# Kernel optimization log

Measured on AMD Instinct MI355X. Metric: run time of the kernel, lower is better.

Reference implementation:

```python
import jax, jax.numpy as jnp
import numpy as np

B, S, T, E = 16, 512, 4096, 256  # batch, phone count, frame count, embed dim


def _pe(t, e):
    # sinusoidal positional encoding table [t, e], matches PositionalEncoding
    pos = jnp.arange(t, dtype=jnp.float32)[:, None]
    div = jnp.exp(jnp.arange(0, e, 2, dtype=jnp.float32) * (-np.log(10000.0) / e))
    pe = jnp.zeros((t, e), jnp.float32)
    pe = pe.at[:, 0::2].set(jnp.sin(pos * div))
    pe = pe.at[:, 1::2].set(jnp.cos(pos * div))
    return pe


def setup_inputs() -> dict:
    key = jax.random.key(0)
    ks = jax.random.split(key, 8)
    encoder_out = jax.random.normal(ks[0], (B, S, E), jnp.float32)
    # text_phone with adjacent values guaranteed distinct (even pos in [0,29), odd in [30,59))
    base = jax.random.randint(ks[1], (B, S), 0, 29)
    off = (jnp.arange(S) % 2) * 30
    text_phone = (base + off[None, :]).astype(jnp.int64)
    dur = T // S
    align_phone = jnp.repeat(text_phone, dur, axis=1)  # [B, T], consistent alignment
    pitch = jax.random.normal(ks[2], (B, T, 1), jnp.float32)
    beats = jax.random.randint(ks[3], (B, T, 1), 0, 2).astype(jnp.int64)
    # learned parameters
    W_pitch = jax.random.normal(ks[4], (1, E), jnp.float32) * 0.02   # fc_pitch
    b_pitch = jnp.zeros((E,), jnp.float32)
    emb_beats = jax.random.normal(ks[5], (2, E), jnp.float32) * 0.02
    W_pos = jax.random.normal(ks[6], (E, E), jnp.float32) * (1.0 / np.sqrt(E))  # fc_pos
    b_pos = jnp.zeros((E,), jnp.float32)
    return dict(encoder_out=encoder_out, align_phone=align_phone, text_phone=text_phone,
                pitch=pitch, beats=beats, W_pitch=W_pitch, b_pitch=b_pitch,
                emb_beats=emb_beats, W_pos=W_pos, b_pos=b_pos)


def _align_indices(align_phone, text_phone):
    # Vectorized version of the serial aligner loop: per batch, an index into
    # encoder_out that stays while align_phone matches the current text phone
    # and advances by 1 otherwise.
    Bb, Ss = text_phone.shape
    barange = jnp.arange(Bb)

    def step(idx, a_j):
        before = text_phone[barange, idx]
        new = jnp.where(a_j == before, idx, jnp.minimum(idx + 1, Ss - 1))
        return new, new

    idx0 = jnp.zeros((Bb,), jnp.int32)
    _, rest = jax.lax.scan(step, idx0, align_phone[:, 1:].T)  # [T-1, B]
    return jnp.concatenate([idx0[None, :], rest], axis=0).T  # [B, T]


def reference(encoder_out, align_phone, text_phone, pitch, beats,
              W_pitch, b_pitch, emb_beats, W_pos, b_pos):
    idx = _align_indices(align_phone, text_phone)                       # [B, T]
    aligner_out = jnp.take_along_axis(encoder_out, idx[:, :, None].astype(jnp.int32), axis=1)  # [B, T, E]
    pitch_emb = pitch @ W_pitch + b_pitch                               # fc_pitch(pitch)
    beat_emb = emb_beats[beats[..., 0]]                                 # emb_beats(beats.squeeze(-1))
    # pos(aligner_out.transpose(0,1)) then transpose back; dropout is identity in eval
    pos_encode = aligner_out + _pe(aligner_out.shape[1], aligner_out.shape[2])[None, :, :]
    pos_out = pos_encode @ W_pos + b_pos                                # fc_pos
    return aligner_out + pitch_emb + beat_emb + pos_out
```

## Files before the change

kernel.cpp:

```cpp
#include <hip/hip_runtime.h>
#include <hip/hip_bf16.h>
#include <math.h>

constexpr int B_ = 16, S_ = 512, T_ = 4096, E_ = 256;

typedef __attribute__((ext_vector_type(8))) short short8;
typedef __attribute__((ext_vector_type(4))) float f32x4;

constexpr size_t FLAGS_OFF = 0;
constexpr size_t WT_OFF    = 4096;

#define NEGC (-0.035977892f)

__device__ __forceinline__ unsigned pk_bf16(float a, float b) {
    __hip_bfloat162 h = __float22bfloat162_rn(make_float2(a, b));
    return *(unsigned*)&h;
}
__device__ __forceinline__ short bf16s(float x) {
    unsigned u = __float_as_uint(x);
    u += 0x7FFFu + ((u >> 16) & 1u);
    return (short)(u >> 16);
}

__global__ __launch_bounds__(256) void k_prep(
    const int* __restrict__ align, const int* __restrict__ text,
    const float* __restrict__ W,
    int* __restrict__ flags, short* __restrict__ wt)
{
    const int bid = blockIdx.x, tid = threadIdx.x;
    if (bid < 32) {
        __shared__ int f;
        if (tid == 0) f = 0;
        __syncthreads();
        const int base = (bid * 256 + tid) * 8;
        const int4 a0 = *(const int4*)(align + base);
        const int4 a1 = *(const int4*)(align + base + 4);
        const int av[8] = {a0.x, a0.y, a0.z, a0.w, a1.x, a1.y, a1.z, a1.w};
        int bad = 0;
#pragma unroll
        for (int m = 0; m < 8; ++m) {
            const int id = base + m;
            const int t = id & (T_ - 1), b = id >> 12;
            if (t > 0) {
                const int prev = (t - 1) >> 3;
                const int expct = (av[m] == text[b * S_ + prev]) ? prev : min(prev + 1, S_ - 1);
                if ((t >> 3) != expct) bad = 1;
            }
        }
        if (bad) f = 1;
        __syncthreads();
        if (tid == 0) flags[bid] = f;
    } else {
        const int kb = (bid - 32) * 16;
        short8 v0, v1;
#pragma unroll
        for (int j = 0; j < 8; ++j) v0[j] = bf16s(W[(kb + j) * E_ + tid]);
#pragma unroll
        for (int j = 0; j < 8; ++j) v1[j] = bf16s(W[(kb + 8 + j) * E_ + tid]);
        *(short8*)(wt + tid * E_ + kb)     = v0;
        *(short8*)(wt + tid * E_ + kb + 8) = v1;
    }
}

__global__ __launch_bounds__(256) void k_fused(
    const float* __restrict__ enc, const short* __restrict__ wt,
    const float* __restrict__ bpos,
    const float* __restrict__ pitch, const int* __restrict__ beats,
    const float* __restrict__ wpitch, const float* __restrict__ bpitch,
    const float* __restrict__ embb,
    const float* __restrict__ W, const int* __restrict__ align,
    const int* __restrict__ text, const int* __restrict__ flags,
    float* __restrict__ out)
{
    __shared__ __align__(16) short As[64 * 256];
    __shared__ __align__(16) short Bs[64 * 256];
    __shared__ float pl[32 * 68];
    __shared__ int idxl[16][32];

    const int tid = threadIdx.x;
    const int i0 = blockIdx.x * 4;
    const int n0 = blockIdx.y * 64;
    const int t0base = i0 * 8;

    const bool fb = __any(flags[tid & 31] != 0);
    if (fb) {
        if (tid < 16) {
            int i = 0;
            const int b = tid;
            if (i0 == 0) idxl[b][0] = 0;
            const int tmax = t0base + 32;
            for (int t = 1; t < tmax; ++t) {
                if (align[b * T_ + t] != text[b * S_ + i]) i = min(i + 1, S_ - 1);
                if (t >= t0base) idxl[b][t - t0base] = i;
            }
        }
        __syncthreads();
        for (int r = tid; r < 512; r += 256) {
            const int bq = r >> 5, tt = r & 31;
            const int t = t0base + tt;
            const int i = idxl[bq][tt];
            const float* erow = enc + (size_t)(bq * S_ + i) * E_;
            const float p = pitch[(size_t)bq * T_ + t];
            const int bt = beats[(size_t)bq * T_ + t];
            for (int cc = 0; cc < 64; ++cc) {
                const int col = n0 + cc;
                float acc = 0.f;
                for (int k2 = 0; k2 < 128; ++k2) {
                    const float d = __expf((float)(2 * k2) * NEGC);
                    float s, c;
                    __sincosf((float)t * d, &s, &c);
                    acc += (erow[2 * k2] + s) * W[(2 * k2) * E_ + col]
                         + (erow[2 * k2 + 1] + c) * W[(2 * k2 + 1) * E_ + col];
                }
                out[((size_t)bq * T_ + t) * E_ + col] =
                    erow[col] + acc + bpos[col] + p * wpitch[col] + bpitch[col]
                    + (bt ? embb[E_ + col] : embb[col]);
            }
        }
        return;
    }

    const int c4o = tid & 15, rg = tid >> 4;
    const int gc = n0 + 4 * c4o;
    const int j = rg & 3;
    const int t0 = t0base + j * 8;
    float4 pi0[4], pi1[4]; int4 bt0[4], bt1[4]; f32x4 e4[4];
#pragma unroll
    for (int p = 0; p < 4; ++p) {
        const int bq = (rg + p * 16) >> 2;
        const size_t prow = (size_t)bq * T_ + t0;
        pi0[p] = *(const float4*)(pitch + prow);
        pi1[p] = *(const float4*)(pitch + prow + 4);
        bt0[p] = *(const int4*)(beats + prow);
        bt1[p] = *(const int4*)(beats + prow + 4);
        e4[p]  = *(const f32x4*)(enc + (size_t)(bq * S_ + i0 + j) * E_ + gc);
    }
    const f32x4 wp4 = *(const f32x4*)(wpitch + gc);
    const f32x4 cst = *(const f32x4*)(bpitch + gc) + *(const f32x4*)(bpos + gc);
    const f32x4 be0 = *(const f32x4*)(embb + gc);
    const f32x4 be1 = *(const f32x4*)(embb + E_ + gc);

    {
        const int r = tid >> 2, c4 = tid & 3;
        const short* bp = wt + (size_t)(n0 + r) * E_;
#pragma unroll
        for (int jj = 0; jj < 8; ++jj) {
            const int seg = c4 + 4 * jj;
            short8 v = *(const short8*)(bp + seg * 8);
            *(short8*)&Bs[(r * 256 + seg * 8) ^ ((r & 7) << 3)] = v;
        }
    }
    {
        const int r = tid >> 3;
        const int c8 = tid & 7;
        const float tf = (float)(t0base + r);
#pragma unroll
        for (int jj = 0; jj < 4; ++jj) {
            const int seg = c8 * 4 + jj;
            union { short8 v; unsigned u[4]; } cv;
#pragma unroll
            for (int m = 0; m < 4; ++m) {
                const int j2 = seg * 4 + m;
                const float d = __expf((float)(2 * j2) * NEGC);
                float s, c;
                __sincosf(tf * d, &s, &c);
                cv.u[m] = pk_bf16(s, c);
            }
            *(short8*)&As[(r * 256 + seg * 8) ^ ((r & 7) << 3)] = cv.v;
        }
    }
    __syncthreads();

    const int wid = tid >> 6, lane = tid & 63;
    const int q = lane >> 4, c = lane & 15;

    {
        const int ar = (wid & 1) * 16 + c;
        const int br0 = (wid >> 1) * 32 + c, br1 = br0 + 16;
        f32x4 p0 = {0.f, 0.f, 0.f, 0.f}, p1 = {0.f, 0.f, 0.f, 0.f};
#pragma unroll
        for (int ks = 0; ks < 8; ++ks) {
            const int kidx = ks * 32 + q * 8;
            short8 a  = *(const short8*)&As[(ar * 256 + kidx) ^ ((ar & 7) << 3)];
            short8 b0 = *(const short8*)&Bs[(br0 * 256 + kidx) ^ ((br0 & 7) << 3)];
            short8 b1 = *(const short8*)&Bs[(br1 * 256 + kidx) ^ ((br1 & 7) << 3)];
            p0 = __builtin_amdgcn_mfma_f32_16x16x32_bf16(a, b0, p0, 0, 0, 0);
            p1 = __builtin_amdgcn_mfma_f32_16x16x32_bf16(a, b1, p1, 0, 0, 0);
        }
#pragma unroll
        for (int rr = 0; rr < 4; ++rr) {
            const int prw = (wid & 1) * 16 + q * 4 + rr;
            pl[prw * 68 + (wid >> 1) * 32 + c]      = p0[rr];
            pl[prw * 68 + (wid >> 1) * 32 + 16 + c] = p1[rr];
        }
    }
    __syncthreads();

    f32x4 pv[8];
    {
        const int r = tid >> 2, c4 = tid & 3;
        const float* ap = enc + (size_t)((r >> 2) * S_ + i0 + (r & 3)) * E_;
#pragma unroll
        for (int jj = 0; jj < 8; ++jj) {
            const int seg = c4 + 4 * jj;
            float4 f0 = *(const float4*)(ap + seg * 8);
            float4 f1 = *(const float4*)(ap + seg * 8 + 4);
            union { short8 v; unsigned u[4]; } cv;
            cv.u[0] = pk_bf16(f0.x, f0.y);
            cv.u[1] = pk_bf16(f0.z, f0.w);
            cv.u[2] = pk_bf16(f1.x, f1.y);
            cv.u[3] = pk_bf16(f1.z, f1.w);
            *(short8*)&As[(r * 256 + seg * 8) ^ ((r & 7) << 3)] = cv.v;
        }
#pragma unroll
        for (int d = 0; d < 8; ++d)
            pv[d] = *(const f32x4*)&pl[(j * 8 + d) * 68 + 4 * c4o];
    }
    __syncthreads();

    const int wm = (wid >> 1) << 5, wn = (wid & 1) << 5;
    f32x4 acc[2][2] = {{{0.f, 0.f, 0.f, 0.f}, {0.f, 0.f, 0.f, 0.f}},
                       {{0.f, 0.f, 0.f, 0.f}, {0.f, 0.f, 0.f, 0.f}}};
#pragma unroll
    for (int ks = 0; ks < 8; ++ks) {
        const int kidx = ks * 32 + q * 8;
        const int ra0 = wm + c, ra1 = wm + 16 + c;
        const int rb0 = wn + c, rb1 = wn + 16 + c;
        short8 a0 = *(const short8*)&As[(ra0 * 256 + kidx) ^ ((ra0 & 7) << 3)];
        short8 a1 = *(const short8*)&As[(ra1 * 256 + kidx) ^ ((ra1 & 7) << 3)];
        short8 b0 = *(const short8*)&Bs[(rb0 * 256 + kidx) ^ ((rb0 & 7) << 3)];
        short8 b1 = *(const short8*)&Bs[(rb1 * 256 + kidx) ^ ((rb1 & 7) << 3)];
        acc[0][0] = __builtin_amdgcn_mfma_f32_16x16x32_bf16(a0, b0, acc[0][0], 0, 0, 0);
        acc[0][1] = __builtin_amdgcn_mfma_f32_16x16x32_bf16(a0, b1, acc[0][1], 0, 0, 0);
        acc[1][0] = __builtin_amdgcn_mfma_f32_16x16x32_bf16(a1, b0, acc[1][0], 0, 0, 0);
        acc[1][1] = __builtin_amdgcn_mfma_f32_16x16x32_bf16(a1, b1, acc[1][1], 0, 0, 0);
    }

    __syncthreads();
    float* ew = (float*)As;
#pragma unroll
    for (int mt = 0; mt < 2; ++mt)
#pragma unroll
        for (int nh = 0; nh < 2; ++nh)
#pragma unroll
            for (int rr = 0; rr < 4; ++rr)
                ew[(wm + mt * 16 + q * 4 + rr) * 68 + wn + nh * 16 + c] = acc[mt][nh][rr];
    __syncthreads();

#pragma unroll
    for (int p = 0; p < 4; ++p) {
        const int lrow = rg + p * 16;
        const int bq = lrow >> 2;
        const f32x4 ewv = *(const f32x4*)&ew[lrow * 68 + 4 * c4o];
        const f32x4 base = ewv + e4[p] + cst;
        const size_t prow = (size_t)bq * T_ + t0;
        const float pp[8] = {pi0[p].x, pi0[p].y, pi0[p].z, pi0[p].w,
                             pi1[p].x, pi1[p].y, pi1[p].z, pi1[p].w};
        const int   bb[8] = {bt0[p].x, bt0[p].y, bt0[p].z, bt0[p].w,
                             bt1[p].x, bt1[p].y, bt1[p].z, bt1[p].w};
#pragma unroll
        for (int d = 0; d < 8; ++d) {
            const f32x4 be = bb[d] ? be1 : be0;
            f32x4 o = base + pv[d] + pp[d] * wp4 + be;
            __builtin_nontemporal_store(o, (f32x4*)(out + (prow + d) * E_ + gc));
        }
    }
}

extern "C" void kernel_launch(void* const* d_in, const int* in_sizes, int n_in,
                              void* d_out, int out_size, void* d_ws, size_t ws_size,
                              hipStream_t stream) {
    const float* enc    = (const float*)d_in[0];
    const int*   align  = (const int*)  d_in[1];
    const int*   text   = (const int*)  d_in[2];
    const float* pitch  = (const float*)d_in[3];
    const int*   beats  = (const int*)  d_in[4];
    const float* wpitch = (const float*)d_in[5];
    const float* bpitch = (const float*)d_in[6];
    const float* embb   = (const float*)d_in[7];
    const float* wpos   = (const float*)d_in[8];
    const float* bpos   = (const float*)d_in[9];
    float* out = (float*)d_out;

    char* ws = (char*)d_ws;
    int*   flags = (int*)  (ws + FLAGS_OFF);
    short* wt    = (short*)(ws + WT_OFF);

    hipLaunchKernelGGL(k_prep, dim3(48), dim3(256), 0, stream,
                       align, text, wpos, flags, wt);
    hipLaunchKernelGGL(k_fused, dim3(S_ / 4, 4), dim3(256), 0, stream,
                       enc, wt, bpos, pitch, beats, wpitch, bpitch, embb,
                       wpos, align, text, flags, out);
}
```

Measured before the change: 26.33 us.

## Precompute positional-encoding projection table in prep kernel, stream A from global

Moves the PE@W_pos (+b_pos) computation out of the fused kernel into extra blocks of the prep kernel. Those blocks build a 4096x256 fp32 table in workspace, which the fused kernel then loads per row. The fused kernel also drops its A-tile LDS staging: it feeds MFMA directly from global encoder rows converted to bf16, which cuts LDS use and a sync. In exchange it adds a 4 MB table write and read through global memory, and prep now launches 304 blocks.

```diff
diff --git a/kernel.cpp b/kernel.cpp
--- a/kernel.cpp
+++ b/kernel.cpp
@@ -9,6 +9,7 @@
 
 constexpr size_t FLAGS_OFF = 0;
 constexpr size_t WT_OFF    = 4096;
+constexpr size_t PEW_OFF   = 256u * 1024;
 
 #define NEGC (-0.035977892f)
 
@@ -24,8 +25,8 @@
 
 __global__ __launch_bounds__(256) void k_prep(
     const int* __restrict__ align, const int* __restrict__ text,
-    const float* __restrict__ W,
-    int* __restrict__ flags, short* __restrict__ wt)
+    const float* __restrict__ W, const float* __restrict__ bpos,
+    int* __restrict__ flags, short* __restrict__ wt, float* __restrict__ pew)
 {
     const int bid = blockIdx.x, tid = threadIdx.x;
     if (bid < 32) {
@@ -50,7 +51,9 @@
         if (bad) f = 1;
         __syncthreads();
         if (tid == 0) flags[bid] = f;
-    } else {
+        return;
+    }
+    if (bid < 48) {
         const int kb = (bid - 32) * 16;
         short8 v0, v1;
 #pragma unroll
@@ -59,23 +62,90 @@
         for (int j = 0; j < 8; ++j) v1[j] = bf16s(W[(kb + 8 + j) * E_ + tid]);
         *(short8*)(wt + tid * E_ + kb)     = v0;
         *(short8*)(wt + tid * E_ + kb + 8) = v1;
-    }
+        return;
+    }
+
+    __shared__ __align__(16) short As[64 * 256];
+    __shared__ __align__(16) short Bs[64 * 256];
+    const int pid = bid - 48;
+    const int m0 = (pid >> 2) * 64;
+    const int n0 = (pid & 3) * 64;
+
+    {
+        const int k = tid;
+        const float* wrow = W + (size_t)k * E_ + n0;
+#pragma unroll
+        for (int jj = 0; jj < 16; ++jj) {
+            const float4 v = *(const float4*)(wrow + jj * 4);
+            const int n = jj * 4;
+            Bs[((n + 0) * 256 + k) ^ (((n + 0) & 7) << 3)] = bf16s(v.x);
+            Bs[((n + 1) * 256 + k) ^ (((n + 1) & 7) << 3)] = bf16s(v.y);
+            Bs[((n + 2) * 256 + k) ^ (((n + 2) & 7) << 3)] = bf16s(v.z);
+            Bs[((n + 3) * 256 + k) ^ (((n + 3) & 7) << 3)] = bf16s(v.w);
+        }
+    }
+    {
+        const int r = tid >> 2, c4 = tid & 3;
+        const float tf = (float)(m0 + r);
+#pragma unroll
+        for (int jj = 0; jj < 8; ++jj) {
+            const int seg = c4 + 4 * jj;
+            union { short8 v; unsigned u[4]; } cv;
+#pragma unroll
+            for (int m = 0; m < 4; ++m) {
+                const int j2 = seg * 4 + m;
+                const float d = __expf((float)(2 * j2) * NEGC);
+                float s, c;
+                __sincosf(tf * d, &s, &c);
+                cv.u[m] = pk_bf16(s, c);
+            }
+            *(short8*)&As[(r * 256 + seg * 8) ^ ((r & 7) << 3)] = cv.v;
+        }
+    }
+    __syncthreads();
+
+    const int wid = tid >> 6, lane = tid & 63;
+    const int q = lane >> 4, c = lane & 15;
+    const int wm = (wid >> 1) << 5, wn = (wid & 1) << 5;
+    f32x4 acc[2][2] = {{{0.f, 0.f, 0.f, 0.f}, {0.f, 0.f, 0.f, 0.f}},
+                       {{0.f, 0.f, 0.f, 0.f}, {0.f, 0.f, 0.f, 0.f}}};
+#pragma unroll
+    for (int ks = 0; ks < 8; ++ks) {
+        const int kidx = ks * 32 + q * 8;
+        const int ra0 = wm + c, ra1 = wm + 16 + c;
+        const int rb0 = wn + c, rb1 = wn + 16 + c;
+        short8 a0 = *(const short8*)&As[(ra0 * 256 + kidx) ^ ((ra0 & 7) << 3)];
+        short8 a1 = *(const short8*)&As[(ra1 * 256 + kidx) ^ ((ra1 & 7) << 3)];
+        short8 b0 = *(const short8*)&Bs[(rb0 * 256 + kidx) ^ ((rb0 & 7) << 3)];
+        short8 b1 = *(const short8*)&Bs[(rb1 * 256 + kidx) ^ ((rb1 & 7) << 3)];
+        acc[0][0] = __builtin_amdgcn_mfma_f32_16x16x32_bf16(a0, b0, acc[0][0], 0, 0, 0);
+        acc[0][1] = __builtin_amdgcn_mfma_f32_16x16x32_bf16(a0, b1, acc[0][1], 0, 0, 0);
+        acc[1][0] = __builtin_amdgcn_mfma_f32_16x16x32_bf16(a1, b0, acc[1][0], 0, 0, 0);
+        acc[1][1] = __builtin_amdgcn_mfma_f32_16x16x32_bf16(a1, b1, acc[1][1], 0, 0, 0);
+    }
+    const int gcol0 = n0 + wn + c, gcol1 = gcol0 + 16;
+    const float bp0 = bpos[gcol0], bp1 = bpos[gcol1];
+#pragma unroll
+    for (int mt = 0; mt < 2; ++mt)
+#pragma unroll
+        for (int rr = 0; rr < 4; ++rr) {
+            const int t = m0 + wm + mt * 16 + q * 4 + rr;
+            pew[(size_t)t * E_ + gcol0] = acc[mt][0][rr] + bp0;
+            pew[(size_t)t * E_ + gcol1] = acc[mt][1][rr] + bp1;
+        }
 }
 
 __global__ __launch_bounds__(256) void k_fused(
     const float* __restrict__ enc, const short* __restrict__ wt,
-    const float* __restrict__ bpos,
+    const float* __restrict__ pew,
     const float* __restrict__ pitch, const int* __restrict__ beats,
     const float* __restrict__ wpitch, const float* __restrict__ bpitch,
     const float* __restrict__ embb,
     const float* __restrict__ W, const int* __restrict__ align,
     const int* __restrict__ text, const int* __restrict__ flags,
-    float* __restrict__ out)
+    const float* __restrict__ bpos, float* __restrict__ out)
 {
-    __shared__ __align__(16) short As[64 * 256];
     __shared__ __align__(16) short Bs[64 * 256];
-    __shared__ float pl[32 * 68];
-    __shared__ int idxl[16][32];
 
     const int tid = threadIdx.x;
     const int i0 = blockIdx.x * 4;
@@ -84,6 +154,7 @@
 
     const bool fb = __any(flags[tid & 31] != 0);
     if (fb) {
+        int (*idxl)[32] = (int(*)[32])Bs;
         if (tid < 16) {
             int i = 0;
             const int b = tid;
@@ -120,144 +191,86 @@
         return;
     }
 
+    {
+        const int r = tid >> 2, c4 = tid & 3;
+        const short* bp = wt + (size_t)(n0 + r) * E_;
+#pragma unroll
+        for (int jj = 0; jj < 8; ++jj) {
+            const int seg = c4 + 4 * jj;
+            short8 v = *(const short8*)(bp + seg * 8);
+            *(short8*)&Bs[(r * 256 + seg * 8) ^ ((r & 7) << 3)] = v;
+        }
+    }
+    __syncthreads();
+
+    const int wid = tid >> 6, lane = tid & 63;
+    const int q = lane >> 4, c = lane & 15;
+    const int wm = (wid >> 1) << 5, wn = (wid & 1) << 5;
+    const int ra0 = wm + c, ra1 = wm + 16 + c;
+    const int rb0 = wn + c, rb1 = wn + 16 + c;
+    const float* ap0 = enc + (size_t)((ra0 >> 2) * S_ + i0 + (ra0 & 3)) * E_;
+    const float* ap1 = enc + (size_t)((ra1 >> 2) * S_ + i0 + (ra1 & 3)) * E_;
+
+    f32x4 acc[2][2] = {{{0.f, 0.f, 0.f, 0.f}, {0.f, 0.f, 0.f, 0.f}},
+                       {{0.f, 0.f, 0.f, 0.f}, {0.f, 0.f, 0.f, 0.f}}};
+#pragma unroll
+    for (int ks = 0; ks < 8; ++ks) {
+        const int kidx = ks * 32 + q * 8;
+        const float4 f0 = *(const float4*)(ap0 + kidx);
+        const float4 f1 = *(const float4*)(ap0 + kidx + 4);
+        const float4 g0 = *(const float4*)(ap1 + kidx);
+        const float4 g1 = *(const float4*)(ap1 + kidx + 4);
+        union { short8 v; unsigned u[4]; } a0, a1;
+        a0.u[0] = pk_bf16(f0.x, f0.y); a0.u[1] = pk_bf16(f0.z, f0.w);
+        a0.u[2] = pk_bf16(f1.x, f1.y); a0.u[3] = pk_bf16(f1.z, f1.w);
+        a1.u[0] = pk_bf16(g0.x, g0.y); a1.u[1] = pk_bf16(g0.z, g0.w);
+        a1.u[2] = pk_bf16(g1.x, g1.y); a1.u[3] = pk_bf16(g1.z, g1.w);
+        short8 b0 = *(const short8*)&Bs[(rb0 * 256 + kidx) ^ ((rb0 & 7) << 3)];
+        short8 b1 = *(const short8*)&Bs[(rb1 * 256 + kidx) ^ ((rb1 & 7) << 3)];
+        acc[0][0] = __builtin_amdgcn_mfma_f32_16x16x32_bf16(a0.v, b0, acc[0][0], 0, 0, 0);
+        acc[0][1] = __builtin_amdgcn_mfma_f32_16x16x32_bf16(a0.v, b1, acc[0][1], 0, 0, 0);
+        acc[1][0] = __builtin_amdgcn_mfma_f32_16x16x32_bf16(a1.v, b0, acc[1][0], 0, 0, 0);
+        acc[1][1] = __builtin_amdgcn_mfma_f32_16x16x32_bf16(a1.v, b1, acc[1][1], 0, 0, 0);
+    }
+
+    __syncthreads();
+    float* ew = (float*)Bs;
+#pragma unroll
+    for (int mt = 0; mt < 2; ++mt)
+#pragma unroll
+        for (int nh = 0; nh < 2; ++nh)
+#pragma unroll
+            for (int rr = 0; rr < 4; ++rr)
+                ew[(wm + mt * 16 + q * 4 + rr) * 68 + wn + nh * 16 + c] = acc[mt][nh][rr];
+
     const int c4o = tid & 15, rg = tid >> 4;
     const int gc = n0 + 4 * c4o;
     const int j = rg & 3;
     const int t0 = t0base + j * 8;
-    float4 pi0[4], pi1[4]; int4 bt0[4], bt1[4]; f32x4 e4[4];
-#pragma unroll
-    for (int p = 0; p < 4; ++p) {
-        const int bq = (rg + p * 16) >> 2;
-        const size_t prow = (size_t)bq * T_ + t0;
-        pi0[p] = *(const float4*)(pitch + prow);
-        pi1[p] = *(const float4*)(pitch + prow + 4);
-        bt0[p] = *(const int4*)(beats + prow);
-        bt1[p] = *(const int4*)(beats + prow + 4);
-        e4[p]  = *(const f32x4*)(enc + (size_t)(bq * S_ + i0 + j) * E_ + gc);
-    }
+    f32x4 pv[8];
+#pragma unroll
+    for (int d = 0; d < 8; ++d)
+        pv[d] = *(const f32x4*)(pew + (size_t)(t0 + d) * E_ + gc);
     const f32x4 wp4 = *(const f32x4*)(wpitch + gc);
-    const f32x4 cst = *(const f32x4*)(bpitch + gc) + *(const f32x4*)(bpos + gc);
+    const f32x4 cst = *(const f32x4*)(bpitch + gc);
     const f32x4 be0 = *(const f32x4*)(embb + gc);
     const f32x4 be1 = *(const f32x4*)(embb + E_ + gc);
-
-    {
-        const int r = tid >> 2, c4 = tid & 3;
-        const short* bp = wt + (size_t)(n0 + r) * E_;
-#pragma unroll
-        for (int jj = 0; jj < 8; ++jj) {
-            const int seg = c4 + 4 * jj;
-            short8 v = *(const short8*)(bp + seg * 8);
-            *(short8*)&Bs[(r * 256 + seg * 8) ^ ((r & 7) << 3)] = v;
-        }
-    }
-    {
-        const int r = tid >> 3;
-        const int c8 = tid & 7;
-        const float tf = (float)(t0base + r);
-#pragma unroll
-        for (int jj = 0; jj < 4; ++jj) {
-            const int seg = c8 * 4 + jj;
-            union { short8 v; unsigned u[4]; } cv;
-#pragma unroll
-            for (int m = 0; m < 4; ++m) {
-                const int j2 = seg * 4 + m;
-                const float d = __expf((float)(2 * j2) * NEGC);
-                float s, c;
-                __sincosf(tf * d, &s, &c);
-                cv.u[m] = pk_bf16(s, c);
-            }
-            *(short8*)&As[(r * 256 + seg * 8) ^ ((r & 7) << 3)] = cv.v;
-        }
-    }
-    __syncthreads();
-
-    const int wid = tid >> 6, lane = tid & 63;
-    const int q = lane >> 4, c = lane & 15;
-
-    {
-        const int ar = (wid & 1) * 16 + c;
-        const int br0 = (wid >> 1) * 32 + c, br1 = br0 + 16;
-        f32x4 p0 = {0.f, 0.f, 0.f, 0.f}, p1 = {0.f, 0.f, 0.f, 0.f};
-#pragma unroll
-        for (int ks = 0; ks < 8; ++ks) {
-            const int kidx = ks * 32 + q * 8;
-            short8 a  = *(const short8*)&As[(ar * 256 + kidx) ^ ((ar & 7) << 3)];
-            short8 b0 = *(const short8*)&Bs[(br0 * 256 + kidx) ^ ((br0 & 7) << 3)];
-            short8 b1 = *(const short8*)&Bs[(br1 * 256 + kidx) ^ ((br1 & 7) << 3)];
-            p0 = __builtin_amdgcn_mfma_f32_16x16x32_bf16(a, b0, p0, 0, 0, 0);
-            p1 = __builtin_amdgcn_mfma_f32_16x16x32_bf16(a, b1, p1, 0, 0, 0);
-        }
-#pragma unroll
-        for (int rr = 0; rr < 4; ++rr) {
-            const int prw = (wid & 1) * 16 + q * 4 + rr;
-            pl[prw * 68 + (wid >> 1) * 32 + c]      = p0[rr];
-            pl[prw * 68 + (wid >> 1) * 32 + 16 + c] = p1[rr];
-        }
-    }
-    __syncthreads();
-
-    f32x4 pv[8];
-    {
-        const int r = tid >> 2, c4 = tid & 3;
-        const float* ap = enc + (size_t)((r >> 2) * S_ + i0 + (r & 3)) * E_;
-#pragma unroll
-        for (int jj = 0; jj < 8; ++jj) {
-            const int seg = c4 + 4 * jj;
-            float4 f0 = *(const float4*)(ap + seg * 8);
-            float4 f1 = *(const float4*)(ap + seg * 8 + 4);
-            union { short8 v; unsigned u[4]; } cv;
-            cv.u[0] = pk_bf16(f0.x, f0.y);
-            cv.u[1] = pk_bf16(f0.z, f0.w);
-            cv.u[2] = pk_bf16(f1.x, f1.y);
-            cv.u[3] = pk_bf16(f1.z, f1.w);
-            *(short8*)&As[(r * 256 + seg * 8) ^ ((r & 7) << 3)] = cv.v;
-        }
-#pragma unroll
-        for (int d = 0; d < 8; ++d)
-            pv[d] = *(const f32x4*)&pl[(j * 8 + d) * 68 + 4 * c4o];
-    }
-    __syncthreads();
-
-    const int wm = (wid >> 1) << 5, wn = (wid & 1) << 5;
-    f32x4 acc[2][2] = {{{0.f, 0.f, 0.f, 0.f}, {0.f, 0.f, 0.f, 0.f}},
-                       {{0.f, 0.f, 0.f, 0.f}, {0.f, 0.f, 0.f, 0.f}}};
-#pragma unroll
-    for (int ks = 0; ks < 8; ++ks) {
-        const int kidx = ks * 32 + q * 8;
-        const int ra0 = wm + c, ra1 = wm + 16 + c;
-        const int rb0 = wn + c, rb1 = wn + 16 + c;
-        short8 a0 = *(const short8*)&As[(ra0 * 256 + kidx) ^ ((ra0 & 7) << 3)];
-        short8 a1 = *(const short8*)&As[(ra1 * 256 + kidx) ^ ((ra1 & 7) << 3)];
-        short8 b0 = *(const short8*)&Bs[(rb0 * 256 + kidx) ^ ((rb0 & 7) << 3)];
-        short8 b1 = *(const short8*)&Bs[(rb1 * 256 + kidx) ^ ((rb1 & 7) << 3)];
-        acc[0][0] = __builtin_amdgcn_mfma_f32_16x16x32_bf16(a0, b0, acc[0][0], 0, 0, 0);
-        acc[0][1] = __builtin_amdgcn_mfma_f32_16x16x32_bf16(a0, b1, acc[0][1], 0, 0, 0);
-        acc[1][0] = __builtin_amdgcn_mfma_f32_16x16x32_bf16(a1, b0, acc[1][0], 0, 0, 0);
-        acc[1][1] = __builtin_amdgcn_mfma_f32_16x16x32_bf16(a1, b1, acc[1][1], 0, 0, 0);
-    }
-
-    __syncthreads();
-    float* ew = (float*)As;
-#pragma unroll
-    for (int mt = 0; mt < 2; ++mt)
-#pragma unroll
-        for (int nh = 0; nh < 2; ++nh)
-#pragma unroll
-            for (int rr = 0; rr < 4; ++rr)
-                ew[(wm + mt * 16 + q * 4 + rr) * 68 + wn + nh * 16 + c] = acc[mt][nh][rr];
     __syncthreads();
 
 #pragma unroll
     for (int p = 0; p < 4; ++p) {
         const int lrow = rg + p * 16;
         const int bq = lrow >> 2;
+        const size_t prow = (size_t)bq * T_ + t0;
+        const float4 pi0 = *(const float4*)(pitch + prow);
+        const float4 pi1 = *(const float4*)(pitch + prow + 4);
+        const int4  bt0 = *(const int4*)(beats + prow);
+        const int4  bt1 = *(const int4*)(beats + prow + 4);
+        const f32x4 e4  = *(const f32x4*)(enc + (size_t)(bq * S_ + i0 + j) * E_ + gc);
         const f32x4 ewv = *(const f32x4*)&ew[lrow * 68 + 4 * c4o];
-        const f32x4 base = ewv + e4[p] + cst;
-        const size_t prow = (size_t)bq * T_ + t0;
-        const float pp[8] = {pi0[p].x, pi0[p].y, pi0[p].z, pi0[p].w,
-                             pi1[p].x, pi1[p].y, pi1[p].z, pi1[p].w};
-        const int   bb[8] = {bt0[p].x, bt0[p].y, bt0[p].z, bt0[p].w,
-                             bt1[p].x, bt1[p].y, bt1[p].z, bt1[p].w};
+        const f32x4 base = ewv + e4 + cst;
+        const float pp[8] = {pi0.x, pi0.y, pi0.z, pi0.w, pi1.x, pi1.y, pi1.z, pi1.w};
+        const int   bb[8] = {bt0.x, bt0.y, bt0.z, bt0.w, bt1.x, bt1.y, bt1.z, bt1.w};
 #pragma unroll
         for (int d = 0; d < 8; ++d) {
             const f32x4 be = bb[d] ? be1 : be0;
@@ -285,10 +298,11 @@
     char* ws = (char*)d_ws;
     int*   flags = (int*)  (ws + FLAGS_OFF);
     short* wt    = (short*)(ws + WT_OFF);
-
-    hipLaunchKernelGGL(k_prep, dim3(48), dim3(256), 0, stream,
-                       align, text, wpos, flags, wt);
+    float* pew   = (float*)(ws + PEW_OFF);
+
+    hipLaunchKernelGGL(k_prep, dim3(304), dim3(256), 0, stream,
+                       align, text, wpos, bpos, flags, wt, pew);
     hipLaunchKernelGGL(k_fused, dim3(S_ / 4, 4), dim3(256), 0, stream,
-                       enc, wt, bpos, pitch, beats, wpitch, bpitch, embb,
-                       wpos, align, text, flags, out);
-}
+                       enc, wt, pew, pitch, beats, wpitch, bpitch, embb,
+                       wpos, align, text, flags, bpos, out);
+}
```

After: 33.26 us. 26.3% more time.

## Shrink per-block tile to one phone per block and quadruple grid size

Applied to the files above, without the earlier changes.

Each block now handles a single phone index (8 frames × 16 batches) instead of four, so the grid grows from 128×4 to 512×4 blocks. Each wave computes one 16×16 MFMA tile instead of four, and shared memory per block drops, which allows more blocks per CU. The epilogue goes through a small per-wave transpose buffer with only a wave-local LDS wait instead of a block-wide barrier. In exchange, the W^T tile is reloaded into LDS by four times as many blocks, and the fallback path is re-split to match.

```diff
diff --git a/kernel.cpp b/kernel.cpp
--- a/kernel.cpp
+++ b/kernel.cpp
@@ -72,73 +72,52 @@
     const int* __restrict__ text, const int* __restrict__ flags,
     float* __restrict__ out)
 {
-    __shared__ __align__(16) short As[64 * 256];
     __shared__ __align__(16) short Bs[64 * 256];
-    __shared__ float pl[32 * 68];
-    __shared__ int idxl[16][32];
+    __shared__ __align__(16) short As[16 * 256];
+    __shared__ float pl[16 * 68];
+    __shared__ float tr[4][16][20];
 
     const int tid = threadIdx.x;
-    const int i0 = blockIdx.x * 4;
+    const int i0 = blockIdx.x;
     const int n0 = blockIdx.y * 64;
-    const int t0base = i0 * 8;
+    const int t0 = i0 * 8;
 
     const bool fb = __any(flags[tid & 31] != 0);
     if (fb) {
+        int (*idxl)[8] = (int(*)[8])As;
         if (tid < 16) {
             int i = 0;
             const int b = tid;
             if (i0 == 0) idxl[b][0] = 0;
-            const int tmax = t0base + 32;
-            for (int t = 1; t < tmax; ++t) {
+            for (int t = 1; t < t0 + 8; ++t) {
                 if (align[b * T_ + t] != text[b * S_ + i]) i = min(i + 1, S_ - 1);
-                if (t >= t0base) idxl[b][t - t0base] = i;
+                if (t >= t0) idxl[b][t - t0] = i;
             }
         }
         __syncthreads();
-        for (int r = tid; r < 512; r += 256) {
-            const int bq = r >> 5, tt = r & 31;
-            const int t = t0base + tt;
-            const int i = idxl[bq][tt];
-            const float* erow = enc + (size_t)(bq * S_ + i) * E_;
-            const float p = pitch[(size_t)bq * T_ + t];
-            const int bt = beats[(size_t)bq * T_ + t];
-            for (int cc = 0; cc < 64; ++cc) {
-                const int col = n0 + cc;
-                float acc = 0.f;
-                for (int k2 = 0; k2 < 128; ++k2) {
-                    const float d = __expf((float)(2 * k2) * NEGC);
-                    float s, c;
-                    __sincosf((float)t * d, &s, &c);
-                    acc += (erow[2 * k2] + s) * W[(2 * k2) * E_ + col]
-                         + (erow[2 * k2 + 1] + c) * W[(2 * k2 + 1) * E_ + col];
-                }
-                out[((size_t)bq * T_ + t) * E_ + col] =
-                    erow[col] + acc + bpos[col] + p * wpitch[col] + bpitch[col]
-                    + (bt ? embb[E_ + col] : embb[col]);
-            }
+        const int r = tid >> 1, half = tid & 1;
+        const int bq = r >> 3, d = r & 7;
+        const int t = t0 + d;
+        const int i = idxl[bq][d];
+        const float* erow = enc + (size_t)(bq * S_ + i) * E_;
+        const float p = pitch[(size_t)bq * T_ + t];
+        const int bt = beats[(size_t)bq * T_ + t];
+        for (int cc = 0; cc < 32; ++cc) {
+            const int col = n0 + half * 32 + cc;
+            float acc = 0.f;
+            for (int k2 = 0; k2 < 128; ++k2) {
+                const float dd = __expf((float)(2 * k2) * NEGC);
+                float s, c;
+                __sincosf((float)t * dd, &s, &c);
+                acc += (erow[2 * k2] + s) * W[(2 * k2) * E_ + col]
+                     + (erow[2 * k2 + 1] + c) * W[(2 * k2 + 1) * E_ + col];
+            }
+            out[((size_t)bq * T_ + t) * E_ + col] =
+                erow[col] + acc + bpos[col] + p * wpitch[col] + bpitch[col]
+                + (bt ? embb[E_ + col] : embb[col]);
         }
         return;
     }
-
-    const int c4o = tid & 15, rg = tid >> 4;
-    const int gc = n0 + 4 * c4o;
-    const int j = rg & 3;
-    const int t0 = t0base + j * 8;
-    float4 pi0[4], pi1[4]; int4 bt0[4], bt1[4]; f32x4 e4[4];
-#pragma unroll
-    for (int p = 0; p < 4; ++p) {
-        const int bq = (rg + p * 16) >> 2;
-        const size_t prow = (size_t)bq * T_ + t0;
-        pi0[p] = *(const float4*)(pitch + prow);
-        pi1[p] = *(const float4*)(pitch + prow + 4);
-        bt0[p] = *(const int4*)(beats + prow);
-        bt1[p] = *(const int4*)(beats + prow + 4);
-        e4[p]  = *(const f32x4*)(enc + (size_t)(bq * S_ + i0 + j) * E_ + gc);
-    }
-    const f32x4 wp4 = *(const f32x4*)(wpitch + gc);
-    const f32x4 cst = *(const f32x4*)(bpitch + gc) + *(const f32x4*)(bpos + gc);
-    const f32x4 be0 = *(const f32x4*)(embb + gc);
-    const f32x4 be1 = *(const f32x4*)(embb + E_ + gc);
 
     {
         const int r = tid >> 2, c4 = tid & 3;
@@ -150,120 +129,101 @@
             *(short8*)&Bs[(r * 256 + seg * 8) ^ ((r & 7) << 3)] = v;
         }
     }
-    {
-        const int r = tid >> 3;
-        const int c8 = tid & 7;
-        const float tf = (float)(t0base + r);
-#pragma unroll
-        for (int jj = 0; jj < 4; ++jj) {
-            const int seg = c8 * 4 + jj;
+    if (tid < 128) {
+        const int r = tid >> 4, c16 = tid & 15;
+        const float tf = (float)(t0 + r);
+#pragma unroll
+        for (int g = 0; g < 2; ++g) {
+            const int k0 = c16 * 16 + g * 8;
             union { short8 v; unsigned u[4]; } cv;
 #pragma unroll
             for (int m = 0; m < 4; ++m) {
-                const int j2 = seg * 4 + m;
+                const int j2 = c16 * 8 + g * 4 + m;
                 const float d = __expf((float)(2 * j2) * NEGC);
                 float s, c;
                 __sincosf(tf * d, &s, &c);
                 cv.u[m] = pk_bf16(s, c);
             }
-            *(short8*)&As[(r * 256 + seg * 8) ^ ((r & 7) << 3)] = cv.v;
+            *(short8*)&As[(r * 256 + k0) ^ ((r & 7) << 3)] = cv.v;
         }
     }
     __syncthreads();
 
     const int wid = tid >> 6, lane = tid & 63;
     const int q = lane >> 4, c = lane & 15;
+    const int rb = wid * 16 + c;
 
     {
-        const int ar = (wid & 1) * 16 + c;
-        const int br0 = (wid >> 1) * 32 + c, br1 = br0 + 16;
-        f32x4 p0 = {0.f, 0.f, 0.f, 0.f}, p1 = {0.f, 0.f, 0.f, 0.f};
+        f32x4 p = {0.f, 0.f, 0.f, 0.f};
 #pragma unroll
         for (int ks = 0; ks < 8; ++ks) {
             const int kidx = ks * 32 + q * 8;
-            short8 a  = *(const short8*)&As[(ar * 256 + kidx) ^ ((ar & 7) << 3)];
-            short8 b0 = *(const short8*)&Bs[(br0 * 256 + kidx) ^ ((br0 & 7) << 3)];
-            short8 b1 = *(const short8*)&Bs[(br1 * 256 + kidx) ^ ((br1 & 7) << 3)];
-            p0 = __builtin_amdgcn_mfma_f32_16x16x32_bf16(a, b0, p0, 0, 0, 0);
-            p1 = __builtin_amdgcn_mfma_f32_16x16x32_bf16(a, b1, p1, 0, 0, 0);
-        }
-#pragma unroll
-        for (int rr = 0; rr < 4; ++rr) {
-            const int prw = (wid & 1) * 16 + q * 4 + rr;
-            pl[prw * 68 + (wid >> 1) * 32 + c]      = p0[rr];
-            pl[prw * 68 + (wid >> 1) * 32 + 16 + c] = p1[rr];
-        }
+            short8 a = *(const short8*)&As[(c * 256 + kidx) ^ ((c & 7) << 3)];
+            short8 b = *(const short8*)&Bs[(rb * 256 + kidx) ^ ((rb & 7) << 3)];
+            p = __builtin_amdgcn_mfma_f32_16x16x32_bf16(a, b, p, 0, 0, 0);
+        }
+#pragma unroll
+        for (int rr = 0; rr < 4; ++rr)
+            pl[(q * 4 + rr) * 68 + wid * 16 + c] = p[rr];
     }
     __syncthreads();
 
-    f32x4 pv[8];
     {
-        const int r = tid >> 2, c4 = tid & 3;
-        const float* ap = enc + (size_t)((r >> 2) * S_ + i0 + (r & 3)) * E_;
-#pragma unroll
-        for (int jj = 0; jj < 8; ++jj) {
-            const int seg = c4 + 4 * jj;
-            float4 f0 = *(const float4*)(ap + seg * 8);
-            float4 f1 = *(const float4*)(ap + seg * 8 + 4);
-            union { short8 v; unsigned u[4]; } cv;
-            cv.u[0] = pk_bf16(f0.x, f0.y);
-            cv.u[1] = pk_bf16(f0.z, f0.w);
-            cv.u[2] = pk_bf16(f1.x, f1.y);
-            cv.u[3] = pk_bf16(f1.z, f1.w);
-            *(short8*)&As[(r * 256 + seg * 8) ^ ((r & 7) << 3)] = cv.v;
-        }
-#pragma unroll
-        for (int d = 0; d < 8; ++d)
-            pv[d] = *(const f32x4*)&pl[(j * 8 + d) * 68 + 4 * c4o];
+        const int r = tid >> 4, c16 = tid & 15;
+        const float* ap = enc + (size_t)(r * S_ + i0) * E_ + c16 * 16;
+        const float4 e0 = *(const float4*)(ap);
+        const float4 e1 = *(const float4*)(ap + 4);
+        const float4 e2 = *(const float4*)(ap + 8);
+        const float4 e3 = *(const float4*)(ap + 12);
+        union { short8 v; unsigned u[4]; } cv0, cv1;
+        cv0.u[0] = pk_bf16(e0.x, e0.y); cv0.u[1] = pk_bf16(e0.z, e0.w);
+        cv0.u[2] = pk_bf16(e1.x, e1.y); cv0.u[3] = pk_bf16(e1.z, e1.w);
+        cv1.u[0] = pk_bf16(e2.x, e2.y); cv1.u[1] = pk_bf16(e2.z, e2.w);
+        cv1.u[2] = pk_bf16(e3.x, e3.y); cv1.u[3] = pk_bf16(e3.z, e3.w);
+        *(short8*)&As[(r * 256 + c16 * 16)     ^ ((r & 7) << 3)] = cv0.v;
+        *(short8*)&As[(r * 256 + c16 * 16 + 8) ^ ((r & 7) << 3)] = cv1.v;
     }
     __syncthreads();
 
-    const int wm = (wid >> 1) << 5, wn = (wid & 1) << 5;
-    f32x4 acc[2][2] = {{{0.f, 0.f, 0.f, 0.f}, {0.f, 0.f, 0.f, 0.f}},
-                       {{0.f, 0.f, 0.f, 0.f}, {0.f, 0.f, 0.f, 0.f}}};
+    f32x4 acc = {0.f, 0.f, 0.f, 0.f};
 #pragma unroll
     for (int ks = 0; ks < 8; ++ks) {
         const int kidx = ks * 32 + q * 8;
-        const int ra0 = wm + c, ra1 = wm + 16 + c;
-        const int rb0 = wn + c, rb1 = wn + 16 + c;
-        short8 a0 = *(const short8*)&As[(ra0 * 256 + kidx) ^ ((ra0 & 7) << 3)];
-        short8 a1 = *(const short8*)&As[(ra1 * 256 + kidx) ^ ((ra1 & 7) << 3)];
-        short8 b0 = *(const short8*)&Bs[(rb0 * 256 + kidx) ^ ((rb0 & 7) << 3)];
-        short8 b1 = *(const short8*)&Bs[(rb1 * 256 + kidx) ^ ((rb1 & 7) << 3)];
-        acc[0][0] = __builtin_amdgcn_mfma_f32_16x16x32_bf16(a0, b0, acc[0][0], 0, 0, 0);
-        acc[0][1] = __builtin_amdgcn_mfma_f32_16x16x32_bf16(a0, b1, acc[0][1], 0, 0, 0);
-        acc[1][0] = __builtin_amdgcn_mfma_f32_16x16x32_bf16(a1, b0, acc[1][0], 0, 0, 0);
-        acc[1][1] = __builtin_amdgcn_mfma_f32_16x16x32_bf16(a1, b1, acc[1][1], 0, 0, 0);
-    }
-
-    __syncthreads();
-    float* ew = (float*)As;
-#pragma unroll
-    for (int mt = 0; mt < 2; ++mt)
-#pragma unroll
-        for (int nh = 0; nh < 2; ++nh)
-#pragma unroll
-            for (int rr = 0; rr < 4; ++rr)
-                ew[(wm + mt * 16 + q * 4 + rr) * 68 + wn + nh * 16 + c] = acc[mt][nh][rr];
-    __syncthreads();
-
-#pragma unroll
-    for (int p = 0; p < 4; ++p) {
-        const int lrow = rg + p * 16;
-        const int bq = lrow >> 2;
-        const f32x4 ewv = *(const f32x4*)&ew[lrow * 68 + 4 * c4o];
-        const f32x4 base = ewv + e4[p] + cst;
-        const size_t prow = (size_t)bq * T_ + t0;
-        const float pp[8] = {pi0[p].x, pi0[p].y, pi0[p].z, pi0[p].w,
-                             pi1[p].x, pi1[p].y, pi1[p].z, pi1[p].w};
-        const int   bb[8] = {bt0[p].x, bt0[p].y, bt0[p].z, bt0[p].w,
-                             bt1[p].x, bt1[p].y, bt1[p].z, bt1[p].w};
-#pragma unroll
-        for (int d = 0; d < 8; ++d) {
-            const f32x4 be = bb[d] ? be1 : be0;
-            f32x4 o = base + pv[d] + pp[d] * wp4 + be;
-            __builtin_nontemporal_store(o, (f32x4*)(out + (prow + d) * E_ + gc));
-        }
+        short8 a = *(const short8*)&As[(c * 256 + kidx) ^ ((c & 7) << 3)];
+        short8 b = *(const short8*)&Bs[(rb * 256 + kidx) ^ ((rb & 7) << 3)];
+        acc = __builtin_amdgcn_mfma_f32_16x16x32_bf16(a, b, acc, 0, 0, 0);
+    }
+
+#pragma unroll
+    for (int rr = 0; rr < 4; ++rr)
+        tr[wid][q * 4 + rr][c] = acc[rr];
+    asm volatile("s_waitcnt lgkmcnt(0)" ::: "memory");
+    __builtin_amdgcn_sched_barrier(0);
+
+    const int r_l = lane >> 2, cq = lane & 3;
+    const int gc = n0 + wid * 16 + cq * 4;
+    const size_t prow = (size_t)r_l * T_ + t0;
+
+    const float4 pi0 = *(const float4*)(pitch + prow);
+    const float4 pi1 = *(const float4*)(pitch + prow + 4);
+    const int4   bt0 = *(const int4*)(beats + prow);
+    const int4   bt1 = *(const int4*)(beats + prow + 4);
+    const f32x4  e4  = *(const f32x4*)(enc + (size_t)(r_l * S_ + i0) * E_ + gc);
+    const f32x4  trv = *(const f32x4*)&tr[wid][r_l][cq * 4];
+    const f32x4  wp4 = *(const f32x4*)(wpitch + gc);
+    const f32x4  cst = *(const f32x4*)(bpitch + gc) + *(const f32x4*)(bpos + gc);
+    const f32x4  be0 = *(const f32x4*)(embb + gc);
+    const f32x4  be1 = *(const f32x4*)(embb + E_ + gc);
+
+    const f32x4 base = trv + e4 + cst;
+    const float pp[8] = {pi0.x, pi0.y, pi0.z, pi0.w, pi1.x, pi1.y, pi1.z, pi1.w};
+    const int   bb[8] = {bt0.x, bt0.y, bt0.z, bt0.w, bt1.x, bt1.y, bt1.z, bt1.w};
+#pragma unroll
+    for (int d = 0; d < 8; ++d) {
+        const f32x4 pv = *(const f32x4*)&pl[d * 68 + wid * 16 + cq * 4];
+        const f32x4 be = bb[d] ? be1 : be0;
+        f32x4 o = base + pv + pp[d] * wp4 + be;
+        __builtin_nontemporal_store(o, (f32x4*)(out + (prow + d) * E_ + gc));
     }
 }
 
@@ -288,7 +248,7 @@
 
     hipLaunchKernelGGL(k_prep, dim3(48), dim3(256), 0, stream,
                        align, text, wpos, flags, wt);
-    hipLaunchKernelGGL(k_fused, dim3(S_ / 4, 4), dim3(256), 0, stream,
+    hipLaunchKernelGGL(k_fused, dim3(512, 4), dim3(256), 0, stream,
                        enc, wt, bpos, pitch, beats, wpitch, bpitch, embb,
                        wpos, align, text, flags, out);
 }
```

Result: slower. 33.60 us (+27.6%).

## Halve output column tile to 32 and shrink LDS for higher occupancy

Applied to the files above, without the earlier changes.

Halves the fused kernel's N tile from 64 to 32 columns and doubles grid.y to 8, giving 1024 blocks. The B tile and partial-sum buffer shrink, the fallback path's index scratch now reuses As, and launch_bounds requests 3 blocks per CU. The pitch, beats and encoder epilogue loads move later to cut register pressure. The cost is that the sinusoid A tile and the encoder rows are now computed or loaded twice as often, once per column tile.

```diff
diff --git a/kernel.cpp b/kernel.cpp
--- a/kernel.cpp
+++ b/kernel.cpp
@@ -62,7 +62,7 @@
     }
 }
 
-__global__ __launch_bounds__(256) void k_fused(
+__global__ __launch_bounds__(256, 3) void k_fused(
     const float* __restrict__ enc, const short* __restrict__ wt,
     const float* __restrict__ bpos,
     const float* __restrict__ pitch, const int* __restrict__ beats,
@@ -73,42 +73,43 @@
     float* __restrict__ out)
 {
     __shared__ __align__(16) short As[64 * 256];
-    __shared__ __align__(16) short Bs[64 * 256];
-    __shared__ float pl[32 * 68];
-    __shared__ int idxl[16][32];
+    __shared__ __align__(16) short Bs[32 * 256];
+    __shared__ float pl[4 * 256];
 
     const int tid = threadIdx.x;
     const int i0 = blockIdx.x * 4;
-    const int n0 = blockIdx.y * 64;
+    const int n0 = blockIdx.y * 32;
     const int t0base = i0 * 8;
 
     const bool fb = __any(flags[tid & 31] != 0);
     if (fb) {
+        int (*idxl)[32] = (int(*)[32])As;
         if (tid < 16) {
             int i = 0;
             const int b = tid;
             if (i0 == 0) idxl[b][0] = 0;
-            const int tmax = t0base + 32;
-            for (int t = 1; t < tmax; ++t) {
+            for (int t = 1; t < t0base + 32; ++t) {
                 if (align[b * T_ + t] != text[b * S_ + i]) i = min(i + 1, S_ - 1);
                 if (t >= t0base) idxl[b][t - t0base] = i;
             }
         }
         __syncthreads();
-        for (int r = tid; r < 512; r += 256) {
+#pragma unroll
+        for (int rr = 0; rr < 2; ++rr) {
+            const int r = tid * 2 + rr;
             const int bq = r >> 5, tt = r & 31;
             const int t = t0base + tt;
             const int i = idxl[bq][tt];
             const float* erow = enc + (size_t)(bq * S_ + i) * E_;
             const float p = pitch[(size_t)bq * T_ + t];
             const int bt = beats[(size_t)bq * T_ + t];
-            for (int cc = 0; cc < 64; ++cc) {
+            for (int cc = 0; cc < 32; ++cc) {
                 const int col = n0 + cc;
                 float acc = 0.f;
                 for (int k2 = 0; k2 < 128; ++k2) {
-                    const float d = __expf((float)(2 * k2) * NEGC);
+                    const float dd = __expf((float)(2 * k2) * NEGC);
                     float s, c;
-                    __sincosf((float)t * d, &s, &c);
+                    __sincosf((float)t * dd, &s, &c);
                     acc += (erow[2 * k2] + s) * W[(2 * k2) * E_ + col]
                          + (erow[2 * k2 + 1] + c) * W[(2 * k2 + 1) * E_ + col];
                 }
@@ -120,39 +121,18 @@
         return;
     }
 
-    const int c4o = tid & 15, rg = tid >> 4;
-    const int gc = n0 + 4 * c4o;
-    const int j = rg & 3;
-    const int t0 = t0base + j * 8;
-    float4 pi0[4], pi1[4]; int4 bt0[4], bt1[4]; f32x4 e4[4];
-#pragma unroll
-    for (int p = 0; p < 4; ++p) {
-        const int bq = (rg + p * 16) >> 2;
-        const size_t prow = (size_t)bq * T_ + t0;
-        pi0[p] = *(const float4*)(pitch + prow);
-        pi1[p] = *(const float4*)(pitch + prow + 4);
-        bt0[p] = *(const int4*)(beats + prow);
-        bt1[p] = *(const int4*)(beats + prow + 4);
-        e4[p]  = *(const f32x4*)(enc + (size_t)(bq * S_ + i0 + j) * E_ + gc);
-    }
-    const f32x4 wp4 = *(const f32x4*)(wpitch + gc);
-    const f32x4 cst = *(const f32x4*)(bpitch + gc) + *(const f32x4*)(bpos + gc);
-    const f32x4 be0 = *(const f32x4*)(embb + gc);
-    const f32x4 be1 = *(const f32x4*)(embb + E_ + gc);
-
-    {
-        const int r = tid >> 2, c4 = tid & 3;
+    {
+        const int r = tid >> 3, c8 = tid & 7;
         const short* bp = wt + (size_t)(n0 + r) * E_;
 #pragma unroll
-        for (int jj = 0; jj < 8; ++jj) {
-            const int seg = c4 + 4 * jj;
+        for (int jj = 0; jj < 4; ++jj) {
+            const int seg = c8 + 8 * jj;
             short8 v = *(const short8*)(bp + seg * 8);
             *(short8*)&Bs[(r * 256 + seg * 8) ^ ((r & 7) << 3)] = v;
         }
     }
     {
-        const int r = tid >> 3;
-        const int c8 = tid & 7;
+        const int r = tid >> 3, c8 = tid & 7;
         const float tf = (float)(t0base + r);
 #pragma unroll
         for (int jj = 0; jj < 4; ++jj) {
@@ -175,28 +155,23 @@
     const int q = lane >> 4, c = lane & 15;
 
     {
-        const int ar = (wid & 1) * 16 + c;
-        const int br0 = (wid >> 1) * 32 + c, br1 = br0 + 16;
-        f32x4 p0 = {0.f, 0.f, 0.f, 0.f}, p1 = {0.f, 0.f, 0.f, 0.f};
+        const int tq = wid >> 1, nqp = wid & 1;
+        const int ar = tq * 16 + c;
+        const int br = nqp * 16 + c;
+        f32x4 p = {0.f, 0.f, 0.f, 0.f};
 #pragma unroll
         for (int ks = 0; ks < 8; ++ks) {
             const int kidx = ks * 32 + q * 8;
-            short8 a  = *(const short8*)&As[(ar * 256 + kidx) ^ ((ar & 7) << 3)];
-            short8 b0 = *(const short8*)&Bs[(br0 * 256 + kidx) ^ ((br0 & 7) << 3)];
-            short8 b1 = *(const short8*)&Bs[(br1 * 256 + kidx) ^ ((br1 & 7) << 3)];
-            p0 = __builtin_amdgcn_mfma_f32_16x16x32_bf16(a, b0, p0, 0, 0, 0);
-            p1 = __builtin_amdgcn_mfma_f32_16x16x32_bf16(a, b1, p1, 0, 0, 0);
-        }
-#pragma unroll
-        for (int rr = 0; rr < 4; ++rr) {
-            const int prw = (wid & 1) * 16 + q * 4 + rr;
-            pl[prw * 68 + (wid >> 1) * 32 + c]      = p0[rr];
-            pl[prw * 68 + (wid >> 1) * 32 + 16 + c] = p1[rr];
-        }
-    }
-    __syncthreads();
-
-    f32x4 pv[8];
+            short8 a = *(const short8*)&As[(ar * 256 + kidx) ^ ((ar & 7) << 3)];
+            short8 b = *(const short8*)&Bs[(br * 256 + kidx) ^ ((br & 7) << 3)];
+            p = __builtin_amdgcn_mfma_f32_16x16x32_bf16(a, b, p, 0, 0, 0);
+        }
+#pragma unroll
+        for (int rr = 0; rr < 4; ++rr)
+            pl[(tq * 2 + nqp) * 256 + (q * 4 + rr) * 16 + c] = p[rr];
+    }
+    __syncthreads();
+
     {
         const int r = tid >> 2, c4 = tid & 3;
         const float* ap = enc + (size_t)((r >> 2) * S_ + i0 + (r & 3)) * E_;
@@ -212,52 +187,61 @@
             cv.u[3] = pk_bf16(f1.z, f1.w);
             *(short8*)&As[(r * 256 + seg * 8) ^ ((r & 7) << 3)] = cv.v;
         }
-#pragma unroll
-        for (int d = 0; d < 8; ++d)
-            pv[d] = *(const f32x4*)&pl[(j * 8 + d) * 68 + 4 * c4o];
-    }
-    __syncthreads();
-
-    const int wm = (wid >> 1) << 5, wn = (wid & 1) << 5;
-    f32x4 acc[2][2] = {{{0.f, 0.f, 0.f, 0.f}, {0.f, 0.f, 0.f, 0.f}},
-                       {{0.f, 0.f, 0.f, 0.f}, {0.f, 0.f, 0.f, 0.f}}};
+    }
+    __syncthreads();
+
+    const int mq = wid >> 1, nq = wid & 1;
+    const int ra0 = mq * 32 + c, ra1 = ra0 + 16;
+    const int rb = nq * 16 + c;
+    f32x4 acc0 = {0.f, 0.f, 0.f, 0.f}, acc1 = {0.f, 0.f, 0.f, 0.f};
 #pragma unroll
     for (int ks = 0; ks < 8; ++ks) {
         const int kidx = ks * 32 + q * 8;
-        const int ra0 = wm + c, ra1 = wm + 16 + c;
-        const int rb0 = wn + c, rb1 = wn + 16 + c;
         short8 a0 = *(const short8*)&As[(ra0 * 256 + kidx) ^ ((ra0 & 7) << 3)];
         short8 a1 = *(const short8*)&As[(ra1 * 256 + kidx) ^ ((ra1 & 7) << 3)];
-        short8 b0 = *(const short8*)&Bs[(rb0 * 256 + kidx) ^ ((rb0 & 7) << 3)];
-        short8 b1 = *(const short8*)&Bs[(rb1 * 256 + kidx) ^ ((rb1 & 7) << 3)];
-        acc[0][0] = __builtin_amdgcn_mfma_f32_16x16x32_bf16(a0, b0, acc[0][0], 0, 0, 0);
-        acc[0][1] = __builtin_amdgcn_mfma_f32_16x16x32_bf16(a0, b1, acc[0][1], 0, 0, 0);
-        acc[1][0] = __builtin_amdgcn_mfma_f32_16x16x32_bf16(a1, b0, acc[1][0], 0, 0, 0);
-        acc[1][1] = __builtin_amdgcn_mfma_f32_16x16x32_bf16(a1, b1, acc[1][1], 0, 0, 0);
-    }
-
-    __syncthreads();
+        short8 b  = *(const short8*)&Bs[(rb * 256 + kidx) ^ ((rb & 7) << 3)];
+        acc0 = __builtin_amdgcn_mfma_f32_16x16x32_bf16(a0, b, acc0, 0, 0, 0);
+        acc1 = __builtin_amdgcn_mfma_f32_16x16x32_bf16(a1, b, acc1, 0, 0, 0);
+    }
+
+    const int c8q = tid & 7, rgrp = tid >> 3;
+    const int j = rgrp & 3;
+    const int gc = n0 + 4 * c8q;
+    f32x4 pv[8];
+#pragma unroll
+    for (int d = 0; d < 8; ++d) {
+        const int tl = j * 8 + d;
+        pv[d] = *(const f32x4*)&pl[((tl >> 4) * 2 + (c8q >> 2)) * 256
+                                   + (tl & 15) * 16 + ((4 * c8q) & 15)];
+    }
+    const f32x4 wp4 = *(const f32x4*)(wpitch + gc);
+    const f32x4 cst = *(const f32x4*)(bpitch + gc) + *(const f32x4*)(bpos + gc);
+    const f32x4 be0 = *(const f32x4*)(embb + gc);
+    const f32x4 be1 = *(const f32x4*)(embb + E_ + gc);
+    __syncthreads();
+
     float* ew = (float*)As;
 #pragma unroll
-    for (int mt = 0; mt < 2; ++mt)
-#pragma unroll
-        for (int nh = 0; nh < 2; ++nh)
-#pragma unroll
-            for (int rr = 0; rr < 4; ++rr)
-                ew[(wm + mt * 16 + q * 4 + rr) * 68 + wn + nh * 16 + c] = acc[mt][nh][rr];
-    __syncthreads();
-
-#pragma unroll
-    for (int p = 0; p < 4; ++p) {
-        const int lrow = rg + p * 16;
-        const int bq = lrow >> 2;
-        const f32x4 ewv = *(const f32x4*)&ew[lrow * 68 + 4 * c4o];
-        const f32x4 base = ewv + e4[p] + cst;
-        const size_t prow = (size_t)bq * T_ + t0;
-        const float pp[8] = {pi0[p].x, pi0[p].y, pi0[p].z, pi0[p].w,
-                             pi1[p].x, pi1[p].y, pi1[p].z, pi1[p].w};
-        const int   bb[8] = {bt0[p].x, bt0[p].y, bt0[p].z, bt0[p].w,
-                             bt1[p].x, bt1[p].y, bt1[p].z, bt1[p].w};
+    for (int rr = 0; rr < 4; ++rr) {
+        ew[(mq * 32 + q * 4 + rr) * 36 + nq * 16 + c]      = acc0[rr];
+        ew[(mq * 32 + 16 + q * 4 + rr) * 36 + nq * 16 + c] = acc1[rr];
+    }
+    __syncthreads();
+
+#pragma unroll
+    for (int p = 0; p < 2; ++p) {
+        const int row = rgrp + 32 * p;
+        const int bq = row >> 2;
+        const size_t prow = (size_t)bq * T_ + t0base + j * 8;
+        const float4 pi0 = *(const float4*)(pitch + prow);
+        const float4 pi1 = *(const float4*)(pitch + prow + 4);
+        const int4  bt0 = *(const int4*)(beats + prow);
+        const int4  bt1 = *(const int4*)(beats + prow + 4);
+        const f32x4 e4  = *(const f32x4*)(enc + (size_t)(bq * S_ + i0 + j) * E_ + gc);
+        const f32x4 ewv = *(const f32x4*)&ew[row * 36 + 4 * c8q];
+        const f32x4 base = ewv + e4 + cst;
+        const float pp[8] = {pi0.x, pi0.y, pi0.z, pi0.w, pi1.x, pi1.y, pi1.z, pi1.w};
+        const int   bb[8] = {bt0.x, bt0.y, bt0.z, bt0.w, bt1.x, bt1.y, bt1.z, bt1.w};
 #pragma unroll
         for (int d = 0; d < 8; ++d) {
             const f32x4 be = bb[d] ? be1 : be0;
@@ -288,7 +272,7 @@
 
     hipLaunchKernelGGL(k_prep, dim3(48), dim3(256), 0, stream,
                        align, text, wpos, flags, wt);
-    hipLaunchKernelGGL(k_fused, dim3(S_ / 4, 4), dim3(256), 0, stream,
+    hipLaunchKernelGGL(k_fused, dim3(S_ / 4, 8), dim3(256), 0, stream,
                        enc, wt, bpos, pitch, beats, wpitch, bpitch, embb,
                        wpos, align, text, flags, out);
 }
```

Result: faster. 25.58 us (-2.8%).
